# Performance work log

Hardware: AMD Instinct MI355X
Metric: run time of the kernel (lower is better)

## Reference

```python
import jax, jax.numpy as jnp
import numpy as np
from jax import lax

# BinarizedConv2d (threshold=False branch): per-direction binary conv.
# Bits {0,1} map to {-1,+1}; output = 2*A - K where A = #bit-agreements
# between the patch and the filter, K = Cin*kH*kW (the 'offset').
# A = 2*sum(x&w) - sum(x) - sum(w) + K  =>  out = 4*xw - 2*sx - 2*sw + K.

D, H, W, CIN = 64, 32, 32, 128
KH = KW = 3
COUT = 128
PAD = 1


def _binconv(x, w):
    # x: [D,H,W,Cin] bool, w: [D,kH,kW,Cin,Cout] with 0/1 float values
    d, h, wd, c = x.shape
    kh, kw, cout = w.shape[1], w.shape[2], w.shape[4]
    K = c * kh * kw  # offset = in_channels * kH * kW
    xf = jnp.transpose(x.astype(w.dtype), (0, 3, 1, 2))  # [D,C,H,W]
    # im2col: [D, C*kH*kW, Ho, Wo], feature index = c*kH*kW + i*kW + j
    patches = lax.conv_general_dilated_patches(
        xf, (kh, kw), (1, 1), [(PAD, PAD), (PAD, PAD)])
    ho, wo = patches.shape[2], patches.shape[3]
    p = patches.reshape(d, c, kh, kw, ho, wo)
    xw = jnp.einsum('dcijhw,dijco->dhwo', p, w)      # sum(x & w)
    sx = p.sum(axis=(1, 2, 3))                        # [D,Ho,Wo]
    sw = w.sum(axis=(1, 2, 3))                        # [D,Cout]
    return 4.0 * xw - 2.0 * sx[..., None] - 2.0 * sw[:, None, None, :] + K


def setup_inputs() -> dict:
    key = jax.random.key(0)
    kx, kw = jax.random.split(key)
    x = jax.random.bernoulli(kx, 0.5, (D, H, W, CIN))
    w = jax.random.bernoulli(kw, 0.5, (D, KH, KW, CIN, COUT)).astype(jnp.float32)
    return {'x': x, 'w': w}


def reference(x, w):
    return _binconv(x, w)  # [D,Ho,Wo,Cout] signed binary conv values
```

## Files before the change

kernel.cpp:

```cpp
#include <hip/hip_runtime.h>
#include <hip/hip_bf16.h>
#include <stdint.h>


#define D_    64
#define H_    32
#define W_    32
#define CIN_  128
#define COUT_ 128
#define KK_   1152

__global__ __launch_bounds__(256) void pack_x_kernel(const int* __restrict__ x,
                                                     uint4* __restrict__ xb) {
    int gid  = blockIdx.x * 256 + threadIdx.x;
    int wave = gid >> 6;
    int lane = threadIdx.x & 63;
    long base = (long)wave * CIN_;
    unsigned long long b0 = __ballot(x[base + lane] != 0);
    unsigned long long b1 = __ballot(x[base + 64 + lane] != 0);
    if (lane == 0) {
        xb[wave] = make_uint4((unsigned)b0, (unsigned)(b0 >> 32),
                              (unsigned)b1, (unsigned)(b1 >> 32));
    }
}

__global__ __launch_bounds__(256) void pack_w_kernel(const float* __restrict__ w,
                                                     uint4* __restrict__ wb) {
    int t  = blockIdx.x * 256 + threadIdx.x;
    int o  = t & 127;
    int dt = t >> 7;
    int d  = dt / 9;
    int tap = dt - d * 9;
    const float* wp = w + (long)dt * (CIN_ * COUT_) + o;
    unsigned w0 = 0, w1 = 0, w2 = 0, w3 = 0;
#pragma unroll
    for (int c = 0; c < 32; ++c)  { if (wp[(long)c * COUT_]         != 0.f) w0 |= 1u << c; }
#pragma unroll
    for (int c = 0; c < 32; ++c)  { if (wp[(long)(c + 32) * COUT_]  != 0.f) w1 |= 1u << c; }
#pragma unroll
    for (int c = 0; c < 32; ++c)  { if (wp[(long)(c + 64) * COUT_]  != 0.f) w2 |= 1u << c; }
#pragma unroll
    for (int c = 0; c < 32; ++c)  { if (wp[(long)(c + 96) * COUT_]  != 0.f) w3 |= 1u << c; }
    wb[(long)(d * COUT_ + o) * 9 + tap] = make_uint4(w0, w1, w2, w3);
}

__global__ __launch_bounds__(256) void binconv_kernel(const uint4* __restrict__ xb,
                                                      const uint4* __restrict__ wb,
                                                      float* __restrict__ out) {
    __shared__ uint4 xbt[4][34];

    int bid  = blockIdx.x;
    int d    = bid >> 4;
    int tile = bid & 15;
    int h0   = tile * 2;
    int tid  = threadIdx.x;
    int o    = tid & 127;
    int grp  = tid >> 7;

    if (tid < 4 * 34) {
        int r  = tid / 34;
        int cc = tid - r * 34;
        int hh = h0 - 1 + r;
        int ww = cc - 1;
        uint4 v = make_uint4(0u, 0u, 0u, 0u);
        if (hh >= 0 && hh < H_ && ww >= 0 && ww < W_)
            v = xb[(long)d * (H_ * W_) + hh * W_ + ww];
        xbt[r][cc] = v;
    }

    uint4 wv[9];
    const uint4* wp = wb + (long)(d * COUT_ + o) * 9;
#pragma unroll
    for (int t = 0; t < 9; ++t) wv[t] = wp[t];

    __syncthreads();

    int h = h0 + grp;
    float* op = out + ((long)d * (H_ * W_) + h * W_) * COUT_ + o;

    for (int iw = 0; iw < W_; ++iw) {
        int pop = 0;
#pragma unroll
        for (int i = 0; i < 3; ++i) {
#pragma unroll
            for (int j = 0; j < 3; ++j) {
                uint4 xa = xbt[grp + i][iw + j];
                uint4 wa = wv[i * 3 + j];
                pop += __popc(xa.x ^ wa.x);
                pop += __popc(xa.y ^ wa.y);
                pop += __popc(xa.z ^ wa.z);
                pop += __popc(xa.w ^ wa.w);
            }
        }
        op[(long)iw * COUT_] = (float)(KK_ - 2 * pop);
    }
}

extern "C" void kernel_launch(void* const* d_in, const int* in_sizes, int n_in,
                              void* d_out, int out_size, void* d_ws, size_t ws_size,
                              hipStream_t stream) {
    const int*   x = (const int*)d_in[0];
    const float* w = (const float*)d_in[1];
    float*       out = (float*)d_out;

    uint4* xb = (uint4*)d_ws;
    uint4* wb = xb + (D_ * H_ * W_);

    pack_x_kernel<<<16384, 256, 0, stream>>>(x, xb);
    pack_w_kernel<<<288, 256, 0, stream>>>(w, wb);
    binconv_kernel<<<1024, 256, 0, stream>>>(xb, wb, out);
}
```

Baseline: 132.1 us.

## Vectorize bit-packing loads and add sliding-window register reuse in binconv

pack_x now loads int4 per lane so one wave packs two positions. It uses an interleaved bit order (bit j of word k holds channel 4j+k). pack_w is split four ways per output channel with the same interleaved channel order, which gives four times more threads and fewer serial loads per thread. The main kernel fully unrolls the width loop and keeps a three-column sliding window of packed x in registers, which cuts shared-memory reads. The cost is higher register pressure and larger code, and x and w must use the same bit permutation to stay correct.

```diff
diff --git a/kernel.cpp b/kernel.cpp
--- a/kernel.cpp
+++ b/kernel.cpp
@@ -12,36 +12,39 @@
 
 __global__ __launch_bounds__(256) void pack_x_kernel(const int* __restrict__ x,
                                                      uint4* __restrict__ xb) {
-    int gid  = blockIdx.x * 256 + threadIdx.x;
-    int wave = gid >> 6;
+    int gid = blockIdx.x * 256 + threadIdx.x;
+    int pos = gid >> 5;
+    int c4  = gid & 31;
+    const int4* xp = (const int4*)(x + (long)pos * CIN_) + c4;
+    int4 v = *xp;
+    unsigned long long b0 = __ballot(v.x != 0);
+    unsigned long long b1 = __ballot(v.y != 0);
+    unsigned long long b2 = __ballot(v.z != 0);
+    unsigned long long b3 = __ballot(v.w != 0);
     int lane = threadIdx.x & 63;
-    long base = (long)wave * CIN_;
-    unsigned long long b0 = __ballot(x[base + lane] != 0);
-    unsigned long long b1 = __ballot(x[base + 64 + lane] != 0);
-    if (lane == 0) {
-        xb[wave] = make_uint4((unsigned)b0, (unsigned)(b0 >> 32),
-                              (unsigned)b1, (unsigned)(b1 >> 32));
-    }
+    if (lane == 0)
+        xb[pos] = make_uint4((unsigned)b0, (unsigned)b1, (unsigned)b2, (unsigned)b3);
+    else if (lane == 32)
+        xb[pos] = make_uint4((unsigned)(b0 >> 32), (unsigned)(b1 >> 32),
+                             (unsigned)(b2 >> 32), (unsigned)(b3 >> 32));
 }
 
 __global__ __launch_bounds__(256) void pack_w_kernel(const float* __restrict__ w,
-                                                     uint4* __restrict__ wb) {
-    int t  = blockIdx.x * 256 + threadIdx.x;
-    int o  = t & 127;
-    int dt = t >> 7;
-    int d  = dt / 9;
-    int tap = dt - d * 9;
+                                                     unsigned* __restrict__ wb) {
+    int t    = blockIdx.x * 256 + threadIdx.x;
+    int o    = t & 127;
+    int rest = t >> 7;
+    int k    = rest & 3;
+    int dt   = rest >> 2;
+    int d    = dt / 9;
+    int tap  = dt - d * 9;
     const float* wp = w + (long)dt * (CIN_ * COUT_) + o;
-    unsigned w0 = 0, w1 = 0, w2 = 0, w3 = 0;
+    unsigned m = 0;
 #pragma unroll
-    for (int c = 0; c < 32; ++c)  { if (wp[(long)c * COUT_]         != 0.f) w0 |= 1u << c; }
-#pragma unroll
-    for (int c = 0; c < 32; ++c)  { if (wp[(long)(c + 32) * COUT_]  != 0.f) w1 |= 1u << c; }
-#pragma unroll
-    for (int c = 0; c < 32; ++c)  { if (wp[(long)(c + 64) * COUT_]  != 0.f) w2 |= 1u << c; }
-#pragma unroll
-    for (int c = 0; c < 32; ++c)  { if (wp[(long)(c + 96) * COUT_]  != 0.f) w3 |= 1u << c; }
-    wb[(long)(d * COUT_ + o) * 9 + tap] = make_uint4(w0, w1, w2, w3);
+    for (int j = 0; j < 32; ++j) {
+        if (wp[(long)(4 * j + k) * COUT_] != 0.f) m |= 1u << j;
+    }
+    wb[(((long)d * COUT_ + o) * 9 + tap) * 4 + k] = m;
 }
 
 __global__ __launch_bounds__(256) void binconv_kernel(const uint4* __restrict__ xb,
@@ -78,35 +81,49 @@
     int h = h0 + grp;
     float* op = out + ((long)d * (H_ * W_) + h * W_) * COUT_ + o;
 
+    uint4 ca[3], cb[3], cc_[3];
+#pragma unroll
+    for (int i = 0; i < 3; ++i) {
+        ca[i] = xbt[grp + i][0];
+        cb[i] = xbt[grp + i][1];
+    }
+
+#pragma unroll
     for (int iw = 0; iw < W_; ++iw) {
+#pragma unroll
+        for (int i = 0; i < 3; ++i) cc_[i] = xbt[grp + i][iw + 2];
         int pop = 0;
 #pragma unroll
         for (int i = 0; i < 3; ++i) {
-#pragma unroll
-            for (int j = 0; j < 3; ++j) {
-                uint4 xa = xbt[grp + i][iw + j];
-                uint4 wa = wv[i * 3 + j];
-                pop += __popc(xa.x ^ wa.x);
-                pop += __popc(xa.y ^ wa.y);
-                pop += __popc(xa.z ^ wa.z);
-                pop += __popc(xa.w ^ wa.w);
-            }
+            uint4 xa;
+            uint4 w0 = wv[i * 3 + 0], w1 = wv[i * 3 + 1], w2 = wv[i * 3 + 2];
+            xa = ca[i];
+            pop += __popc(xa.x ^ w0.x) + __popc(xa.y ^ w0.y)
+                 + __popc(xa.z ^ w0.z) + __popc(xa.w ^ w0.w);
+            xa = cb[i];
+            pop += __popc(xa.x ^ w1.x) + __popc(xa.y ^ w1.y)
+                 + __popc(xa.z ^ w1.z) + __popc(xa.w ^ w1.w);
+            xa = cc_[i];
+            pop += __popc(xa.x ^ w2.x) + __popc(xa.y ^ w2.y)
+                 + __popc(xa.z ^ w2.z) + __popc(xa.w ^ w2.w);
         }
         op[(long)iw * COUT_] = (float)(KK_ - 2 * pop);
+#pragma unroll
+        for (int i = 0; i < 3; ++i) { ca[i] = cb[i]; cb[i] = cc_[i]; }
     }
 }
 
 extern "C" void kernel_launch(void* const* d_in, const int* in_sizes, int n_in,
                               void* d_out, int out_size, void* d_ws, size_t ws_size,
                               hipStream_t stream) {
-    const int*   x = (const int*)d_in[0];
-    const float* w = (const float*)d_in[1];
+    const int*   x   = (const int*)d_in[0];
+    const float* w   = (const float*)d_in[1];
     float*       out = (float*)d_out;
 
-    uint4* xb = (uint4*)d_ws;
-    uint4* wb = xb + (D_ * H_ * W_);
+    uint4*    xb = (uint4*)d_ws;
+    unsigned* wb = (unsigned*)(xb + (D_ * H_ * W_));
 
-    pack_x_kernel<<<16384, 256, 0, stream>>>(x, xb);
-    pack_w_kernel<<<288, 256, 0, stream>>>(w, wb);
-    binconv_kernel<<<1024, 256, 0, stream>>>(xb, wb, out);
+    pack_x_kernel<<<8192, 256, 0, stream>>>(x, xb);
+    pack_w_kernel<<<1152, 256, 0, stream>>>(w, wb);
+    binconv_kernel<<<1024, 256, 0, stream>>>(xb, (const uint4*)wb, out);
 }
```

Result: faster. 128.5 us (-2.7%).
